# Kernel tuning notes

Hardware: AMD Instinct MI355X
Metric: run time of the kernel (lower is better)

The kernel has to match this reference:

```python
import jax, jax.numpy as jnp
import numpy as np

B, L, DIM, H = 4, 2048, 768, 12
C = DIM // H  # head_dim = 64


def setup_inputs() -> dict:
    key = jax.random.key(0)
    k1, k2, k3 = jax.random.split(key, 3)
    x = jax.random.normal(k1, (B, L, DIM), dtype=jnp.float32)
    # qkv Linear: torch uniform init +-sqrt(6/(dim + 3*dim... per code: out//3 + in))
    val_qkv = np.sqrt(6.0 / float(DIM + DIM))
    Wqkv = jax.random.uniform(k2, (DIM, 3 * DIM), dtype=jnp.float32,
                              minval=-val_qkv, maxval=val_qkv)  # [in, out]
    # proj_out Linear: xavier uniform, bias zeros
    val_o = np.sqrt(6.0 / float(DIM + DIM))
    Wo = jax.random.uniform(k3, (DIM, DIM), dtype=jnp.float32,
                            minval=-val_o, maxval=val_o)  # [in, out]
    bo = jnp.zeros((DIM,), dtype=jnp.float32)
    return {"x": x, "Wqkv": Wqkv, "Wo": Wo, "bo": bo}


def reference(x, Wqkv, Wo, bo):
    b, l, d = x.shape
    qkv = x @ Wqkv                                   # [B, L, 3*dim] (qkv_bias=False)
    qkv = qkv.reshape(b, l, 3, H, C)                 # three interleaved as (three H C)
    q, k, v = qkv[:, :, 0], qkv[:, :, 1], qkv[:, :, 2]  # each [B, L, H, C]
    # NOTE: original forward never applies self.scale -> unscaled dot products
    dots = jnp.einsum('bqhc,bkhc->bhqk', q, k)       # [B, H, L, L]
    attn = jax.nn.softmax(dots, axis=-1)             # attn_drop = 0 -> identity
    out = jnp.einsum('bhqk,bkhc->bqhc', attn, v)     # [B, L, H, C]
    out = out.reshape(b, l, d)                       # (H C) -> dim
    return out @ Wo + bo                             # proj_drop = 0 -> identity
```

## Files before the change

kernel.cpp:

```cpp
#include <hip/hip_runtime.h>
#include <hip/hip_bf16.h>


typedef unsigned short u16;
typedef u16 u16x2 __attribute__((ext_vector_type(2)));
typedef u16 u16x4 __attribute__((ext_vector_type(4)));
typedef u16 u16x8 __attribute__((ext_vector_type(8)));
typedef short bf16x8 __attribute__((ext_vector_type(8)));
typedef float f32x4 __attribute__((ext_vector_type(4)));

#define MFMA16(acc, a, b) \
  asm("v_mfma_f32_16x16x32_bf16 %0, %1, %2, %0" : "+v"(acc) : "v"(a), "v"(b))

__device__ __forceinline__ u16 f2b(float f) {
  unsigned u = __float_as_uint(f);
  return (u16)((u + 0x7fffu + ((u >> 16) & 1u)) >> 16);
}
__device__ __forceinline__ float b2f(u16 h) {
  return __uint_as_float(((unsigned)h) << 16);
}
__device__ __forceinline__ unsigned pk_bf16(float a, float b) {
  unsigned d;
  asm("v_cvt_pk_bf16_f32 %0, %1, %2" : "=v"(d) : "v"(a), "v"(b));
  return d;
}

__device__ __forceinline__ void gload16(const u16* g, u16* l) {
  __builtin_amdgcn_global_load_lds(
      (const __attribute__((address_space(1))) unsigned*)g,
      (__attribute__((address_space(3))) unsigned*)l, 16, 0, 0);
}

__global__ __launch_bounds__(256) void prep_x_kernel(
    const float* __restrict__ X, u16* __restrict__ Xh, u16* __restrict__ Xl) {
  const size_t i = ((size_t)blockIdx.x * 256 + threadIdx.x) * 4;
  float4 v = *(const float4*)(X + i);
  u16 h0 = f2b(v.x), h1 = f2b(v.y), h2 = f2b(v.z), h3 = f2b(v.w);
  u16x4 hs = { h0, h1, h2, h3 };
  u16x4 ls = { f2b(v.x - b2f(h0)), f2b(v.y - b2f(h1)),
               f2b(v.z - b2f(h2)), f2b(v.w - b2f(h3)) };
  *(u16x4*)(Xh + i) = hs;
  *(u16x4*)(Xl + i) = ls;
}

__global__ __launch_bounds__(256) void prep_w_kernel(
    const float* __restrict__ W, u16* __restrict__ WtH, u16* __restrict__ WtL,
    int K, int N) {
  __shared__ float T[32][33];
  const int k0 = blockIdx.x * 32, n0 = blockIdx.y * 32;
  const int tx = threadIdx.x & 31, ty = threadIdx.x >> 5;
  #pragma unroll
  for (int i = 0; i < 4; ++i)
    T[ty + i * 8][tx] = W[(size_t)(k0 + ty + i * 8) * N + n0 + tx];
  __syncthreads();
  #pragma unroll
  for (int i = 0; i < 4; ++i) {
    const int rn = ty + i * 8, ck = tx;
    float v = T[ck][rn];
    u16 h = f2b(v);
    WtH[(size_t)(n0 + rn) * K + k0 + ck] = h;
    WtL[(size_t)(n0 + rn) * K + k0 + ck] = f2b(v - b2f(h));
  }
}

__global__ __launch_bounds__(256) void prep_wo_kernel(
    const float* __restrict__ W, u16* __restrict__ Wt, int K, int N) {
  __shared__ float T[32][33];
  const int k0 = blockIdx.x * 32, n0 = blockIdx.y * 32;
  const int tx = threadIdx.x & 31, ty = threadIdx.x >> 5;
  #pragma unroll
  for (int i = 0; i < 4; ++i)
    T[ty + i * 8][tx] = W[(size_t)(k0 + ty + i * 8) * N + n0 + tx];
  __syncthreads();
  #pragma unroll
  for (int i = 0; i < 4; ++i) {
    const int rn = ty + i * 8, ck = tx;
    Wt[(size_t)(n0 + rn) * K + k0 + ck] = f2b(T[ck][rn]);
  }
}

__global__ __launch_bounds__(256) void qkv_gemm_kernel(
    const u16* __restrict__ Xh, const u16* __restrict__ Xl,
    const u16* __restrict__ WtH, const u16* __restrict__ WtL,
    float* __restrict__ Qo, u16* __restrict__ Ko, u16* __restrict__ Vo) {
  __shared__ u16 Ah[4096], Al[4096], Bh[4096], Bl[4096];
  const int tid = threadIdx.x;
  const int w = tid >> 6, l = tid & 63;
  const int llo = l & 15, lhi = l >> 4;
  const int m0 = blockIdx.x * 128, n0 = blockIdx.y * 128;
  const int t = blockIdx.y / 6;
  const int wr = (w >> 1) * 64, wc = (w & 1) * 64;

  f32x4 acc[4][4] = {};

  const int sr = tid >> 2;
  const int sc = (tid & 3) * 8;
  const unsigned lb = ((unsigned)w) * 512;
  const u16* axh = Xh + (size_t)(m0 + sr) * 768 + sc;
  const u16* axl = Xl + (size_t)(m0 + sr) * 768 + sc;
  const u16* bwh = WtH + (size_t)(n0 + sr) * 768 + sc;
  const u16* bwl = WtL + (size_t)(n0 + sr) * 768 + sc;
  const size_t half = (size_t)64 * 768;

  if (t < 2) {
    for (int k0 = 0; k0 < 768; k0 += 32) {
      __syncthreads();
      gload16(axh + k0,        Ah + lb);
      gload16(axh + half + k0, Ah + 2048 + lb);
      gload16(axl + k0,        Al + lb);
      gload16(axl + half + k0, Al + 2048 + lb);
      gload16(bwh + k0,        Bh + lb);
      gload16(bwh + half + k0, Bh + 2048 + lb);
      gload16(bwl + k0,        Bl + lb);
      gload16(bwl + half + k0, Bl + 2048 + lb);
      __syncthreads();
      bf16x8 ahf[4], alf[4], bhf[4], blf[4];
      #pragma unroll
      for (int i = 0; i < 4; ++i) {
        ahf[i] = *(const bf16x8*)&Ah[(wr + i * 16 + llo) * 32 + lhi * 8];
        alf[i] = *(const bf16x8*)&Al[(wr + i * 16 + llo) * 32 + lhi * 8];
      }
      #pragma unroll
      for (int n = 0; n < 4; ++n) {
        bhf[n] = *(const bf16x8*)&Bh[(wc + n * 16 + llo) * 32 + lhi * 8];
        blf[n] = *(const bf16x8*)&Bl[(wc + n * 16 + llo) * 32 + lhi * 8];
      }
      #pragma unroll
      for (int i = 0; i < 4; ++i)
        #pragma unroll
        for (int n = 0; n < 4; ++n) {
          MFMA16(acc[i][n], ahf[i], bhf[n]);
          MFMA16(acc[i][n], alf[i], bhf[n]);
          MFMA16(acc[i][n], ahf[i], blf[n]);
        }
    }
  } else {
    for (int k0 = 0; k0 < 768; k0 += 32) {
      __syncthreads();
      gload16(axh + k0,        Ah + lb);
      gload16(axh + half + k0, Ah + 2048 + lb);
      gload16(bwh + k0,        Bh + lb);
      gload16(bwh + half + k0, Bh + 2048 + lb);
      __syncthreads();
      bf16x8 ahf[4], bhf[4];
      #pragma unroll
      for (int i = 0; i < 4; ++i)
        ahf[i] = *(const bf16x8*)&Ah[(wr + i * 16 + llo) * 32 + lhi * 8];
      #pragma unroll
      for (int n = 0; n < 4; ++n)
        bhf[n] = *(const bf16x8*)&Bh[(wc + n * 16 + llo) * 32 + lhi * 8];
      #pragma unroll
      for (int i = 0; i < 4; ++i)
        #pragma unroll
        for (int n = 0; n < 4; ++n)
          MFMA16(acc[i][n], ahf[i], bhf[n]);
    }
  }

  #pragma unroll
  for (int i = 0; i < 4; ++i) {
    #pragma unroll
    for (int n = 0; n < 4; ++n) {
      const int gc = n0 + wc + n * 16 + llo;
      const int rem = gc - t * 768;
      const int h = rem >> 6, c = rem & 63;
      #pragma unroll
      for (int r = 0; r < 4; ++r) {
        const int row = m0 + wr + i * 16 + lhi * 4 + r;
        const int b = row >> 11, lq = row & 2047;
        const size_t bh_ = (size_t)(b * 12 + h);
        const float fv = acc[i][n][r];
        if (t == 0)      Qo[(bh_ * 2048 + lq) * 64 + c] = fv;
        else if (t == 1) Ko[(bh_ * 2048 + lq) * 64 + c] = f2b(fv);
        else             Vo[(bh_ * 64 + c) * 2048 + lq] = f2b(fv);
      }
    }
  }
}

__global__ __launch_bounds__(256, 3) void attn_kernel(
    const float* __restrict__ Qf, const u16* __restrict__ Km,
    const u16* __restrict__ Vt, u16* __restrict__ AO) {
  __shared__ u16 Ks[64][72];
  __shared__ u16 Vs[64][72];
  __shared__ u16 Ps[4][32][72];
  const int tid = threadIdx.x;
  const int w = tid >> 6, l = tid & 63;
  const int llo = l & 15, lhi = l >> 4;
  const int id0 = blockIdx.y * 16 + blockIdx.x;
  const int swz = (id0 & 7) * 96 + (id0 >> 3);
  const int bh = swz >> 4;
  const int q0w = (swz & 15) * 128 + w * 32;

  const int kr = tid >> 2, chs = (tid & 3) * 16;
  const u16* Kp = Km + ((size_t)bh * 2048 + kr) * 64 + chs;
  const u16* Vp = Vt + ((size_t)bh * 64 + kr) * 2048 + chs;

  bf16x8 qh[2][2], ql[2][2];
  #pragma unroll
  for (int s = 0; s < 2; ++s) {
    const float* Qp = Qf + ((size_t)bh * 2048 + q0w + s * 16 + llo) * 64 + lhi * 8;
    #pragma unroll
    for (int j = 0; j < 8; ++j) {
      float a = Qp[j], b = Qp[32 + j];
      u16 ha = f2b(a), hb = f2b(b);
      qh[s][0][j] = (short)ha; ql[s][0][j] = (short)f2b(a - b2f(ha));
      qh[s][1][j] = (short)hb; ql[s][1][j] = (short)f2b(b - b2f(hb));
    }
  }

  const float L2E = 1.4426950408889634f;
  float mrow[2] = { -1e30f, -1e30f };
  float lsum[2] = { 0.f, 0.f };
  f32x4 o_acc[2][4] = {};

  {
    u16x8 k0 = *(const u16x8*)(Kp),     k1 = *(const u16x8*)(Kp + 8);
    u16x8 v0 = *(const u16x8*)(Vp),     v1 = *(const u16x8*)(Vp + 8);
    *(u16x8*)&Ks[kr][chs] = k0;  *(u16x8*)&Ks[kr][chs + 8] = k1;
    *(u16x8*)&Vs[kr][chs] = v0;  *(u16x8*)&Vs[kr][chs + 8] = v1;
  }
  __syncthreads();

  for (int kt = 0; kt < 32; ++kt) {
    u16x8 nk0, nk1, nv0, nv1;
    if (kt < 31) {
      const u16* kp = Kp + (size_t)(kt + 1) * 4096;
      const u16* vp = Vp + (size_t)(kt + 1) * 64;
      nk0 = *(const u16x8*)(kp);      nk1 = *(const u16x8*)(kp + 8);
      nv0 = *(const u16x8*)(vp);      nv1 = *(const u16x8*)(vp + 8);
    }

    f32x4 s_acc[2][4] = {};
    #pragma unroll
    for (int kb4 = 0; kb4 < 4; ++kb4) {
      bf16x8 kf0 = *(const bf16x8*)&Ks[kb4 * 16 + llo][lhi * 8];
      bf16x8 kf1 = *(const bf16x8*)&Ks[kb4 * 16 + llo][32 + lhi * 8];
      #pragma unroll
      for (int s = 0; s < 2; ++s) {
        MFMA16(s_acc[s][kb4], kf0, qh[s][0]);
        MFMA16(s_acc[s][kb4], kf0, ql[s][0]);
        MFMA16(s_acc[s][kb4], kf1, qh[s][1]);
        MFMA16(s_acc[s][kb4], kf1, ql[s][1]);
      }
    }

    float tm[2];
    #pragma unroll
    for (int s = 0; s < 2; ++s) {
      float a = fmaxf(fmaxf(s_acc[s][0][0], s_acc[s][0][1]), fmaxf(s_acc[s][0][2], s_acc[s][0][3]));
      float b = fmaxf(fmaxf(s_acc[s][1][0], s_acc[s][1][1]), fmaxf(s_acc[s][1][2], s_acc[s][1][3]));
      float c = fmaxf(fmaxf(s_acc[s][2][0], s_acc[s][2][1]), fmaxf(s_acc[s][2][2], s_acc[s][2][3]));
      float d = fmaxf(fmaxf(s_acc[s][3][0], s_acc[s][3][1]), fmaxf(s_acc[s][3][2], s_acc[s][3][3]));
      tm[s] = fmaxf(fmaxf(a, b), fmaxf(c, d));
    }

    if (!__all(tm[0] <= mrow[0] + 8.f && tm[1] <= mrow[1] + 8.f)) {
      #pragma unroll
      for (int s = 0; s < 2; ++s) {
        float g = tm[s];
        g = fmaxf(g, __shfl_xor(g, 16));
        g = fmaxf(g, __shfl_xor(g, 32));
        const float mn = fmaxf(mrow[s], g);
        const float scale = __expf(mrow[s] - mn);
        mrow[s] = mn;
        lsum[s] *= scale;
        float scr[4];
        #pragma unroll
        for (int r = 0; r < 4; ++r) scr[r] = __shfl(scale, lhi * 20 + r);
        #pragma unroll
        for (int cb = 0; cb < 4; ++cb)
          #pragma unroll
          for (int r = 0; r < 4; ++r) o_acc[s][cb][r] *= scr[r];
      }
    }

    #pragma unroll
    for (int s = 0; s < 2; ++s) {
      const float mb = mrow[s] * L2E;
      float rs = 0.f;
      #pragma unroll
      for (int kb4 = 0; kb4 < 4; ++kb4) {
        float p0 = exp2f(fmaf(s_acc[s][kb4][0], L2E, -mb));
        float p1 = exp2f(fmaf(s_acc[s][kb4][1], L2E, -mb));
        float p2 = exp2f(fmaf(s_acc[s][kb4][2], L2E, -mb));
        float p3 = exp2f(fmaf(s_acc[s][kb4][3], L2E, -mb));
        rs += (p0 + p1) + (p2 + p3);
        uint2 pk = { pk_bf16(p0, p1), pk_bf16(p2, p3) };
        *(uint2*)&Ps[w][s * 16 + llo][kb4 * 16 + lhi * 4] = pk;
      }
      lsum[s] += rs;
    }

    bf16x8 pa[2][2];
    #pragma unroll
    for (int s = 0; s < 2; ++s) {
      pa[s][0] = *(const bf16x8*)&Ps[w][s * 16 + llo][lhi * 8];
      pa[s][1] = *(const bf16x8*)&Ps[w][s * 16 + llo][32 + lhi * 8];
    }
    #pragma unroll
    for (int cb = 0; cb < 4; ++cb) {
      bf16x8 vf0 = *(const bf16x8*)&Vs[cb * 16 + llo][lhi * 8];
      bf16x8 vf1 = *(const bf16x8*)&Vs[cb * 16 + llo][32 + lhi * 8];
      #pragma unroll
      for (int s = 0; s < 2; ++s) {
        MFMA16(o_acc[s][cb], pa[s][0], vf0);
        MFMA16(o_acc[s][cb], pa[s][1], vf1);
      }
    }

    __syncthreads();
    if (kt < 31) {
      *(u16x8*)&Ks[kr][chs] = nk0;  *(u16x8*)&Ks[kr][chs + 8] = nk1;
      *(u16x8*)&Vs[kr][chs] = nv0;  *(u16x8*)&Vs[kr][chs + 8] = nv1;
    }
    __syncthreads();
  }

  const int b = bh / 12, h = bh % 12;
  #pragma unroll
  for (int s = 0; s < 2; ++s) {
    lsum[s] += __shfl_xor(lsum[s], 16);
    lsum[s] += __shfl_xor(lsum[s], 32);
    float ls[4];
    #pragma unroll
    for (int r = 0; r < 4; ++r) ls[r] = __shfl(lsum[s], lhi * 20 + r);
    #pragma unroll
    for (int cb = 0; cb < 4; ++cb)
      #pragma unroll
      for (int r = 0; r < 4; ++r) {
        const float val = o_acc[s][cb][r] / ls[r];
        AO[((size_t)(b * 2048 + q0w + s * 16 + lhi * 4 + r)) * 768 + h * 64 + cb * 16 + llo] = f2b(val);
      }
  }
}

__global__ __launch_bounds__(256) void out_gemm_kernel(
    const u16* __restrict__ A, const u16* __restrict__ Wot,
    const float* __restrict__ bias, float* __restrict__ Out) {
  __shared__ u16 As[4096], Bs[4096];
  const int tid = threadIdx.x;
  const int w = tid >> 6, l = tid & 63;
  const int llo = l & 15, lhi = l >> 4;
  const int m0 = blockIdx.x * 128, n0 = blockIdx.y * 128;
  const int wr = (w >> 1) * 64, wc = (w & 1) * 64;

  f32x4 acc[4][4] = {};

  const int sr = tid >> 2;
  const int sc = (tid & 3) * 8;
  const unsigned lb = ((unsigned)w) * 512;
  const u16* ap = A   + (size_t)(m0 + sr) * 768 + sc;
  const u16* bp = Wot + (size_t)(n0 + sr) * 768 + sc;
  const size_t half = (size_t)64 * 768;

  for (int k0 = 0; k0 < 768; k0 += 32) {
    __syncthreads();
    gload16(ap + k0,        As + lb);
    gload16(ap + half + k0, As + 2048 + lb);
    gload16(bp + k0,        Bs + lb);
    gload16(bp + half + k0, Bs + 2048 + lb);
    __syncthreads();
    bf16x8 af[4], bfr[4];
    #pragma unroll
    for (int i = 0; i < 4; ++i)
      af[i] = *(const bf16x8*)&As[(wr + i * 16 + llo) * 32 + lhi * 8];
    #pragma unroll
    for (int n = 0; n < 4; ++n)
      bfr[n] = *(const bf16x8*)&Bs[(wc + n * 16 + llo) * 32 + lhi * 8];
    #pragma unroll
    for (int i = 0; i < 4; ++i)
      #pragma unroll
      for (int n = 0; n < 4; ++n)
        MFMA16(acc[i][n], af[i], bfr[n]);
  }

  #pragma unroll
  for (int i = 0; i < 4; ++i)
    #pragma unroll
    for (int n = 0; n < 4; ++n) {
      const int gc = n0 + wc + n * 16 + llo;
      const float bb = bias[gc];
      #pragma unroll
      for (int r = 0; r < 4; ++r) {
        const int row = m0 + wr + i * 16 + lhi * 4 + r;
        Out[(size_t)row * 768 + gc] = acc[i][n][r] + bb;
      }
    }
}

extern "C" void kernel_launch(void* const* d_in, const int* in_sizes, int n_in,
                              void* d_out, int out_size, void* d_ws, size_t ws_size,
                              hipStream_t stream) {
  const float* x    = (const float*)d_in[0];
  const float* Wqkv = (const float*)d_in[1];
  const float* Wo   = (const float*)d_in[2];
  const float* bo   = (const float*)d_in[3];
  float* out = (float*)d_out;

  const size_t SEG = (size_t)48 * 2048 * 64;
  float* qf  = (float*)d_ws;
  u16* kk    = (u16*)(qf + SEG);
  u16* vt    = kk + SEG;
  u16* xh    = vt + SEG;
  u16* xl    = xh + SEG;
  u16* wth   = xl + SEG;
  u16* wtl   = wth + (size_t)2304 * 768;
  u16* wot   = wtl + (size_t)2304 * 768;
  u16* ao    = xh;

  prep_x_kernel <<<dim3(6144), 256, 0, stream>>>(x, xh, xl);
  prep_w_kernel <<<dim3(24, 72), 256, 0, stream>>>(Wqkv, wth, wtl, 768, 2304);
  prep_wo_kernel<<<dim3(24, 24), 256, 0, stream>>>(Wo, wot, 768, 768);
  qkv_gemm_kernel<<<dim3(64, 18), 256, 0, stream>>>(xh, xl, wth, wtl, qf, kk, vt);
  attn_kernel   <<<dim3(16, 48), 256, 0, stream>>>(qf, kk, vt, ao);
  out_gemm_kernel<<<dim3(64, 6), 256, 0, stream>>>(ao, wot, bo, out);
}
```

Baseline: 235.8 us.

## Double-buffer K/V shared tiles and XOR-swizzle LDS layout in attention

```diff
diff --git a/kernel.cpp b/kernel.cpp
--- a/kernel.cpp
+++ b/kernel.cpp
@@ -181,20 +181,24 @@
 __global__ __launch_bounds__(256, 3) void attn_kernel(
     const float* __restrict__ Qf, const u16* __restrict__ Km,
     const u16* __restrict__ Vt, u16* __restrict__ AO) {
-  __shared__ u16 Ks[64][72];
-  __shared__ u16 Vs[64][72];
-  __shared__ u16 Ps[4][32][72];
+  __shared__ u16 KsB[2][64 * 64];
+  __shared__ u16 VsB[2][64 * 64];
+  __shared__ u16 PsB[4][32 * 64];
   const int tid = threadIdx.x;
   const int w = tid >> 6, l = tid & 63;
   const int llo = l & 15, lhi = l >> 4;
   const int id0 = blockIdx.y * 16 + blockIdx.x;
-  const int swz = (id0 & 7) * 96 + (id0 >> 3);
-  const int bh = swz >> 4;
-  const int q0w = (swz & 15) * 128 + w * 32;
-
-  const int kr = tid >> 2, chs = (tid & 3) * 16;
-  const u16* Kp = Km + ((size_t)bh * 2048 + kr) * 64 + chs;
-  const u16* Vp = Vt + ((size_t)bh * 64 + kr) * 2048 + chs;
+  const int swzb = (id0 & 7) * 96 + (id0 >> 3);
+  const int bh = swzb >> 4;
+  const int q0w = (swzb & 15) * 128 + w * 32;
+
+  const int sw = (llo & 7) << 4;
+  const int kr = tid >> 2;
+  const int cs = (tid & 3) * 32;
+  const int swk = (kr & 7) << 4;
+  const int c0 = cs ^ swk, c1 = (cs ^ 16) ^ swk;
+  const u16* Kp = Km + ((size_t)bh * 2048 + kr) * 64 + (tid & 3) * 16;
+  const u16* Vp = Vt + ((size_t)bh * 64 + kr) * 2048 + (tid & 3) * 16;
 
   bf16x8 qh[2][2], ql[2][2];
   #pragma unroll
@@ -213,29 +217,35 @@
   float mrow[2] = { -1e30f, -1e30f };
   float lsum[2] = { 0.f, 0.f };
   f32x4 o_acc[2][4] = {};
+  char* const pb = (char*)PsB[w];
 
   {
-    u16x8 k0 = *(const u16x8*)(Kp),     k1 = *(const u16x8*)(Kp + 8);
-    u16x8 v0 = *(const u16x8*)(Vp),     v1 = *(const u16x8*)(Vp + 8);
-    *(u16x8*)&Ks[kr][chs] = k0;  *(u16x8*)&Ks[kr][chs + 8] = k1;
-    *(u16x8*)&Vs[kr][chs] = v0;  *(u16x8*)&Vs[kr][chs + 8] = v1;
+    u16x8 a = *(const u16x8*)(Kp), b = *(const u16x8*)(Kp + 8);
+    u16x8 c = *(const u16x8*)(Vp), d = *(const u16x8*)(Vp + 8);
+    char* kb = (char*)KsB[0];  char* vb = (char*)VsB[0];
+    *(u16x8*)(kb + kr * 128 + c0) = a;  *(u16x8*)(kb + kr * 128 + c1) = b;
+    *(u16x8*)(vb + kr * 128 + c0) = c;  *(u16x8*)(vb + kr * 128 + c1) = d;
   }
   __syncthreads();
 
   for (int kt = 0; kt < 32; ++kt) {
+    const int cur = kt & 1;
+    char* const kb = (char*)KsB[cur];
+    char* const vb = (char*)VsB[cur];
     u16x8 nk0, nk1, nv0, nv1;
     if (kt < 31) {
       const u16* kp = Kp + (size_t)(kt + 1) * 4096;
       const u16* vp = Vp + (size_t)(kt + 1) * 64;
-      nk0 = *(const u16x8*)(kp);      nk1 = *(const u16x8*)(kp + 8);
-      nv0 = *(const u16x8*)(vp);      nv1 = *(const u16x8*)(vp + 8);
+      nk0 = *(const u16x8*)(kp);  nk1 = *(const u16x8*)(kp + 8);
+      nv0 = *(const u16x8*)(vp);  nv1 = *(const u16x8*)(vp + 8);
     }
 
     f32x4 s_acc[2][4] = {};
     #pragma unroll
     for (int kb4 = 0; kb4 < 4; ++kb4) {
-      bf16x8 kf0 = *(const bf16x8*)&Ks[kb4 * 16 + llo][lhi * 8];
-      bf16x8 kf1 = *(const bf16x8*)&Ks[kb4 * 16 + llo][32 + lhi * 8];
+      const int row = kb4 * 16 + llo;
+      bf16x8 kf0 = *(const bf16x8*)(kb + row * 128 + ((lhi * 16) ^ sw));
+      bf16x8 kf1 = *(const bf16x8*)(kb + row * 128 + ((64 + lhi * 16) ^ sw));
       #pragma unroll
       for (int s = 0; s < 2; ++s) {
         MFMA16(s_acc[s][kb4], kf0, qh[s][0]);
@@ -279,6 +289,7 @@
     for (int s = 0; s < 2; ++s) {
       const float mb = mrow[s] * L2E;
       float rs = 0.f;
+      const int rq = s * 16 + llo;
       #pragma unroll
       for (int kb4 = 0; kb4 < 4; ++kb4) {
         float p0 = exp2f(fmaf(s_acc[s][kb4][0], L2E, -mb));
@@ -287,7 +298,7 @@
         float p3 = exp2f(fmaf(s_acc[s][kb4][3], L2E, -mb));
         rs += (p0 + p1) + (p2 + p3);
         uint2 pk = { pk_bf16(p0, p1), pk_bf16(p2, p3) };
-        *(uint2*)&Ps[w][s * 16 + llo][kb4 * 16 + lhi * 4] = pk;
+        *(uint2*)(pb + rq * 128 + ((kb4 * 32 + lhi * 8) ^ sw)) = pk;
       }
       lsum[s] += rs;
     }
@@ -295,13 +306,15 @@
     bf16x8 pa[2][2];
     #pragma unroll
     for (int s = 0; s < 2; ++s) {
-      pa[s][0] = *(const bf16x8*)&Ps[w][s * 16 + llo][lhi * 8];
-      pa[s][1] = *(const bf16x8*)&Ps[w][s * 16 + llo][32 + lhi * 8];
+      const int rq = s * 16 + llo;
+      pa[s][0] = *(const bf16x8*)(pb + rq * 128 + ((lhi * 16) ^ sw));
+      pa[s][1] = *(const bf16x8*)(pb + rq * 128 + ((64 + lhi * 16) ^ sw));
     }
     #pragma unroll
     for (int cb = 0; cb < 4; ++cb) {
-      bf16x8 vf0 = *(const bf16x8*)&Vs[cb * 16 + llo][lhi * 8];
-      bf16x8 vf1 = *(const bf16x8*)&Vs[cb * 16 + llo][32 + lhi * 8];
+      const int row = cb * 16 + llo;
+      bf16x8 vf0 = *(const bf16x8*)(vb + row * 128 + ((lhi * 16) ^ sw));
+      bf16x8 vf1 = *(const bf16x8*)(vb + row * 128 + ((64 + lhi * 16) ^ sw));
       #pragma unroll
       for (int s = 0; s < 2; ++s) {
         MFMA16(o_acc[s][cb], pa[s][0], vf0);
@@ -309,10 +322,10 @@
       }
     }
 
-    __syncthreads();
     if (kt < 31) {
-      *(u16x8*)&Ks[kr][chs] = nk0;  *(u16x8*)&Ks[kr][chs + 8] = nk1;
-      *(u16x8*)&Vs[kr][chs] = nv0;  *(u16x8*)&Vs[kr][chs + 8] = nv1;
+      char* kn = (char*)KsB[cur ^ 1];  char* vn = (char*)VsB[cur ^ 1];
+      *(u16x8*)(kn + kr * 128 + c0) = nk0;  *(u16x8*)(kn + kr * 128 + c1) = nk1;
+      *(u16x8*)(vn + kr * 128 + c0) = nv0;  *(u16x8*)(vn + kr * 128 + c1) = nv1;
     }
     __syncthreads();
   }
```

Result: no change. 235.3 us (median of 2 runs) (-0.2%).
